# Kernel tuning notes

Measured on AMD Instinct MI355X. Metric: run time of the kernel, lower is better.

Reference implementation:

```python
import jax, jax.numpy as jnp
import numpy as np

N = 8192        # num_drugs
D_EMB = 256     # args.gcn_hidden3 (global encoder input)
D_FEAT = 256    # args.hidden_size (local encoder input)
H1 = H2 = H3 = 256  # args.ff_hidden1/2/3
LOG2 = float(np.log(2.0))
ADJ_DENSITY = 0.01


def _ff(x, w1, b1, w2, b2, w3, b3, ws, bs):
    # FF block: 3-layer ReLU MLP + linear shortcut (FF_local / FF_global)
    h = jax.nn.relu(x @ w1 + b1)
    h = jax.nn.relu(h @ w2 + b2)
    h = jax.nn.relu(h @ w3 + b3)
    return h + x @ ws + bs


def _lin_init(k, fan_in, fan_out):
    s = 1.0 / np.sqrt(fan_in)
    kw, kb = jax.random.split(k)
    w = jax.random.uniform(kw, (fan_in, fan_out), minval=-s, maxval=s, dtype=jnp.float32)
    b = jax.random.uniform(kb, (fan_out,), minval=-s, maxval=s, dtype=jnp.float32)
    return w, b


def setup_inputs() -> dict:
    key = jax.random.key(0)
    ks = jax.random.split(key, 11)
    g_w1, g_b1 = _lin_init(ks[0], D_EMB, H1)
    g_w2, g_b2 = _lin_init(ks[1], H1, H2)
    g_w3, g_b3 = _lin_init(ks[2], H2, H3)
    g_ws, g_bs = _lin_init(ks[3], D_EMB, H3)
    l_w1, l_b1 = _lin_init(ks[4], D_FEAT, H1)
    l_w2, l_b2 = _lin_init(ks[5], H1, H2)
    l_w3, l_b3 = _lin_init(ks[6], H2, H3)
    l_ws, l_bs = _lin_init(ks[7], D_FEAT, H3)
    embeddings = jax.random.normal(ks[8], (N, D_EMB), dtype=jnp.float32)
    features = jax.random.normal(ks[9], (N, D_FEAT), dtype=jnp.float32)
    adj_tensor = (jax.random.uniform(ks[10], (N, N)) < ADJ_DENSITY).astype(jnp.float32)
    return dict(embeddings=embeddings, features=features, adj_tensor=adj_tensor,
                num_drugs=N,
                g_w1=g_w1, g_b1=g_b1, g_w2=g_w2, g_b2=g_b2, g_w3=g_w3, g_b3=g_b3,
                g_ws=g_ws, g_bs=g_bs,
                l_w1=l_w1, l_b1=l_b1, l_w2=l_w2, l_b2=l_b2, l_w3=l_w3, l_b3=l_b3,
                l_ws=l_ws, l_bs=l_bs)


def reference(embeddings, features, adj_tensor,
              g_w1, g_b1, g_w2, g_b2, g_w3, g_b3, g_ws, g_bs,
              l_w1, l_b1, l_w2, l_b2, l_w3, l_b3, l_ws, l_bs,
              num_drugs):
    g_enc = _ff(embeddings, g_w1, g_b1, g_w2, g_b2, g_w3, g_b3, g_ws, g_bs)  # [N, H3]
    l_enc = _ff(features,   l_w1, l_b1, l_w2, l_b2, l_w3, l_b3, l_ws, l_bs)  # [N, H3]
    res = l_enc @ g_enc.T                      # [N, N] pairwise local-global scores
    pos_mask = adj_tensor
    neg_mask = 1.0 - adj_tensor
    # JSD estimator (as in InfoGraph/MIRACLE: mask applied BEFORE the expectation)
    p = res * pos_mask
    E_pos = jnp.sum(LOG2 - jax.nn.softplus(-p)) / num_drugs
    q = res * neg_mask
    E_neg = jnp.sum(jax.nn.softplus(-q) + q - LOG2) / (num_drugs * (num_drugs - 1))
    return E_neg - E_pos  # prior=False -> PRIOR term is 0
```

## Files before the change

kernel.cpp:

```cpp
#include <hip/hip_runtime.h>
#include <hip/hip_bf16.h>
#include <stdint.h>

typedef __bf16 bf16;
typedef __bf16 bf16x8 __attribute__((ext_vector_type(8)));
typedef float f32x4 __attribute__((ext_vector_type(4)));

#define N_DRUGS 8192
#define DIM 256
#define LOG2_C 0.6931471805599453f
#define W_POS (1.0f / 8192.0f)
#define W_NEG (1.0f / (8192.0f * 8191.0f))

__device__ inline void gload_lds16(const void* g, void* l) {
  __builtin_amdgcn_global_load_lds(
      (const __attribute__((address_space(1))) void*)g,
      (__attribute__((address_space(3))) void*)l, 16, 0, 0);
}

__device__ inline int swz(int row, int c) {
  return (c & ~7) | ((c ^ row) & 7);
}

__device__ inline float load_as_f32(const void* p, size_t idx, int dt_bf16) {
  return dt_bf16 ? (float)((const bf16*)p)[idx] : ((const float*)p)[idx];
}

__global__ void detect_dtype(const unsigned short* emb, int* flag) {
  int l = threadIdx.x & 63;
  unsigned short u = emb[2 * l];
  int e = (u >> 7) & 0xFF;
  int plausible = (e >= 96 && e <= 140) || (u == 0);
  unsigned long long m = __ballot(plausible);
  if (l == 0) *flag = (__popcll(m) >= 32) ? 1 : 0;
}

struct P8 { const void* p[8]; };

__global__ __launch_bounds__(256) void transpose_w(P8 srcs, bf16* wt,
                                                   const int* flag) {
  __shared__ bf16 t[32][33];
  const int dt = *flag;
  int m = blockIdx.z;
  const void* src = srcs.p[m];
  bf16* dst = wt + m * 65536;
  int bx = blockIdx.x * 32;
  int by = blockIdx.y * 32;
  int tx = threadIdx.x, ty = threadIdx.y;
#pragma unroll
  for (int i = 0; i < 32; i += 8)
    t[ty + i][tx] = (bf16)load_as_f32(src, (size_t)(by + ty + i) * DIM + bx + tx, dt);
  __syncthreads();
#pragma unroll
  for (int i = 0; i < 32; i += 8)
    dst[(bx + ty + i) * DIM + by + tx] = t[tx][ty + i];
}

struct FFArgs {
  const void *x, *b1, *b2, *b3, *bs;
  const bf16 *wt1, *wt2, *wt3, *wts;
  bf16* out;
};
struct FFBoth { FFArgs a[2]; };

__global__ __launch_bounds__(512) void ff_kernel(FFBoth both, const int* flag) {
  __shared__ __align__(16) bf16 xin[64 * 256];
  __shared__ __align__(16) bf16 cur[64 * 256];
  const FFArgs A = (blockIdx.y == 0) ? both.a[0] : both.a[1];
  const int dt = *flag;

  const int t = threadIdx.x;
  const int w = t >> 6, l = t & 63;
  const int lm = l & 15, lq = l >> 4;
  const int n0 = w * 32;
  const int r0 = blockIdx.x * 64;

  if (dt) {
#pragma unroll
    for (int it = 0; it < 4; ++it) {
      int ci = it * 512 + t, row = ci >> 5, c = ci & 31;
      *(bf16x8*)&xin[row * 256 + swz(row, c) * 8] =
          *(const bf16x8*)&((const bf16*)A.x)[(size_t)(r0 + row) * DIM + c * 8];
    }
  } else {
#pragma unroll
    for (int it = 0; it < 4; ++it) {
      int ci = it * 512 + t, row = ci >> 5, c = ci & 31;
      const float* src = &((const float*)A.x)[(size_t)(r0 + row) * DIM + c * 8];
      bf16x8 v;
#pragma unroll
      for (int e = 0; e < 8; ++e) v[e] = (bf16)src[e];
      *(bf16x8*)&xin[row * 256 + swz(row, c) * 8] = v;
    }
  }
  __syncthreads();

  f32x4 acc[4][2];
  const f32x4 fz = {0.f, 0.f, 0.f, 0.f};

  auto compute = [&](const bf16* src, const bf16* wt) {
#pragma unroll
    for (int i = 0; i < 4; ++i)
#pragma unroll
      for (int j = 0; j < 2; ++j) acc[i][j] = fz;
#pragma unroll
    for (int ks = 0; ks < 256; ks += 32) {
      bf16x8 af[4], bfr[2];
#pragma unroll
      for (int i = 0; i < 4; ++i) {
        int row = i * 16 + lm;
        af[i] = *(const bf16x8*)&src[row * 256 + swz(row, (ks >> 3) + lq) * 8];
      }
#pragma unroll
      for (int j = 0; j < 2; ++j) {
        int n = n0 + j * 16 + lm;
        bfr[j] = *(const bf16x8*)&wt[n * DIM + ks + lq * 8];
      }
#pragma unroll
      for (int i = 0; i < 4; ++i)
#pragma unroll
        for (int j = 0; j < 2; ++j)
          acc[i][j] = __builtin_amdgcn_mfma_f32_16x16x32_bf16(af[i], bfr[j],
                                                              acc[i][j], 0, 0, 0);
    }
  };

  auto store_relu = [&](const void* bias) {
    __syncthreads();
#pragma unroll
    for (int j = 0; j < 2; ++j) {
      int col = n0 + j * 16 + lm;
      float bj = load_as_f32(bias, col, dt);
      int cc = col >> 3, cw = col & 7;
#pragma unroll
      for (int i = 0; i < 4; ++i)
#pragma unroll
        for (int r = 0; r < 4; ++r) {
          int row = i * 16 + lq * 4 + r;
          float v = fmaxf(acc[i][j][r] + bj, 0.f);
          cur[row * 256 + swz(row, cc) * 8 + cw] = (bf16)v;
        }
    }
    __syncthreads();
  };

  compute(xin, A.wt1); store_relu(A.b1);
  compute(cur, A.wt2); store_relu(A.b2);
  compute(cur, A.wt3); store_relu(A.b3);
  compute(xin, A.wts);

  __syncthreads();
#pragma unroll
  for (int j = 0; j < 2; ++j) {
    int col = n0 + j * 16 + lm;
    float bj = load_as_f32(A.bs, col, dt);
    int cc = col >> 3, cw = col & 7;
#pragma unroll
    for (int i = 0; i < 4; ++i)
#pragma unroll
      for (int r = 0; r < 4; ++r) {
        int row = i * 16 + lq * 4 + r;
        float h3 = (float)cur[row * 256 + swz(row, cc) * 8 + cw];
        float v = acc[i][j][r] + bj + h3;
        xin[row * 256 + swz(row, cc) * 8 + cw] = (bf16)v;
      }
  }
  __syncthreads();
#pragma unroll
  for (int it = 0; it < 4; ++it) {
    int ci = it * 512 + t, row = ci >> 5, c = ci & 31;
    *(bf16x8*)&A.out[(size_t)(r0 + row) * DIM + c * 8] =
        *(const bf16x8*)&xin[row * 256 + swz(row, c) * 8];
  }
}

__global__ __launch_bounds__(256, 4) void gemm_reduce(const bf16* __restrict__ Lenc,
                                                      const bf16* __restrict__ Genc,
                                                      const void* __restrict__ adj,
                                                      float* accum, const int* flag) {
  __shared__ __align__(16) bf16 sb[2][2][128 * 32];
  __shared__ float red[4];

  const int dt = *flag;
  const int t = threadIdx.x;
  const int w = t >> 6, l = t & 63;
  const int wr = w >> 1, wc = w & 1;
  const int lm = l & 15, lq = l >> 4;
  const int row0 = blockIdx.y * 128;
  const int col0 = blockIdx.x * 128;

  auto stage = [&](int buf, int k) {
#pragma unroll
    for (int q = 0; q < 2; ++q) {
      int ci = q * 256 + t;
      int row = ci >> 2, c = ci & 3;
      int cg = c ^ (row & 3);
      gload_lds16(&Lenc[(size_t)(row0 + row) * DIM + k * 32 + cg * 8],
                  &sb[buf][0][(q * 256 + w * 64) * 8]);
      gload_lds16(&Genc[(size_t)(col0 + row) * DIM + k * 32 + cg * 8],
                  &sb[buf][1][(q * 256 + w * 64) * 8]);
    }
  };

  f32x4 acc[4][4];
  const f32x4 fz = {0.f, 0.f, 0.f, 0.f};
#pragma unroll
  for (int i = 0; i < 4; ++i)
#pragma unroll
    for (int j = 0; j < 4; ++j) acc[i][j] = fz;

  auto compute = [&](int buf) {
    bf16x8 af[4], bfr[4];
#pragma unroll
    for (int i = 0; i < 4; ++i) {
      int row = wr * 64 + i * 16 + lm;
      af[i] = *(const bf16x8*)&sb[buf][0][row * 32 + (lq ^ (row & 3)) * 8];
    }
#pragma unroll
    for (int j = 0; j < 4; ++j) {
      int row = wc * 64 + j * 16 + lm;
      bfr[j] = *(const bf16x8*)&sb[buf][1][row * 32 + (lq ^ (row & 3)) * 8];
    }
#pragma unroll
    for (int i = 0; i < 4; ++i)
#pragma unroll
      for (int j = 0; j < 4; ++j)
        acc[i][j] = __builtin_amdgcn_mfma_f32_16x16x32_bf16(af[i], bfr[j],
                                                            acc[i][j], 0, 0, 0);
  };

  stage(0, 0);
#pragma unroll
  for (int k = 0; k < 8; ++k) {
    const int cur = k & 1;
    if (k < 7) {
      stage(cur ^ 1, k + 1);
      asm volatile("s_waitcnt vmcnt(4)" ::: "memory");
    } else {
      asm volatile("s_waitcnt vmcnt(0)" ::: "memory");
    }
    __builtin_amdgcn_sched_barrier(0);
    __builtin_amdgcn_s_barrier();
    asm volatile("" ::: "memory");
    compute(cur);
    asm volatile("" ::: "memory");
    __builtin_amdgcn_s_barrier();
    asm volatile("" ::: "memory");
  }

  auto jsd = [&](float res, float a) {
    float s = fmaxf(res, 0.f) + __logf(1.f + __expf(-fabsf(res)));
    float vneg = (s - LOG2_C) * W_NEG;
    float vpos = (s - res - LOG2_C) * W_POS;
    return (a > 0.5f) ? vpos : vneg;
  };

  float lsum = 0.f;
  if (dt) {
    const bf16* gsrc = (const bf16*)adj +
        (size_t)(row0 + wr * 64) * N_DRUGS + col0 + wc * 64;
    bf16* wb = (bf16*)sb + w * 4096;
    int r8 = l >> 3, c8 = l & 7;
#pragma unroll
    for (int q = 0; q < 8; ++q)
      gload_lds16(gsrc + (size_t)(q * 8 + r8) * N_DRUGS + c8 * 8, wb + q * 512);
    asm volatile("s_waitcnt vmcnt(0)" ::: "memory");
    __builtin_amdgcn_sched_barrier(0);
#pragma unroll
    for (int i = 0; i < 4; ++i)
#pragma unroll
      for (int r = 0; r < 4; ++r) {
        int rc = i * 16 + lq * 4 + r;
#pragma unroll
        for (int j = 0; j < 4; ++j)
          lsum += jsd(acc[i][j][r], (float)wb[rc * 64 + j * 16 + lm]);
      }
  } else {
    const float* gsrc = (const float*)adj +
        (size_t)(row0 + wr * 64) * N_DRUGS + col0 + wc * 64;
    float* wfb = (float*)sb + w * 2048;
    auto issue = [&](int i) {
      float* cb = wfb + (i & 1) * 1024;
      const float* g = gsrc + (size_t)i * 16 * N_DRUGS;
#pragma unroll
      for (int q = 0; q < 4; ++q)
        gload_lds16(g + (size_t)(q * 4 + lq) * N_DRUGS + lm * 4, cb + q * 256);
    };
    issue(0);
    issue(1);
#pragma unroll
    for (int i = 0; i < 4; ++i) {
      if (i < 3) asm volatile("s_waitcnt vmcnt(4)" ::: "memory");
      else       asm volatile("s_waitcnt vmcnt(0)" ::: "memory");
      __builtin_amdgcn_sched_barrier(0);
      const float* cb = wfb + (i & 1) * 1024;
#pragma unroll
      for (int r = 0; r < 4; ++r) {
        int rc = lq * 4 + r;
#pragma unroll
        for (int j = 0; j < 4; ++j)
          lsum += jsd(acc[i][j][r], cb[rc * 64 + j * 16 + lm]);
      }
      if (i < 2) {
        asm volatile("s_waitcnt lgkmcnt(0)" ::: "memory");
        __builtin_amdgcn_sched_barrier(0);
        issue(i + 2);
      }
    }
  }

#pragma unroll
  for (int off = 32; off > 0; off >>= 1) lsum += __shfl_down(lsum, off, 64);
  if (l == 0) red[w] = lsum;
  __syncthreads();
  if (t == 0) atomicAdd(accum, red[0] + red[1] + red[2] + red[3]);
}

__global__ void finalize_k(const float* accum, unsigned int* out) {
  if (threadIdx.x == 0 && blockIdx.x == 0) {
    float v = *accum;
    union { bf16 h; unsigned short u; } cv;
    cv.h = (bf16)v;
    out[0] = ((unsigned int)cv.u << 16) | cv.u;
  }
}

extern "C" void kernel_launch(void* const* d_in, const int* in_sizes, int n_in,
                              void* d_out, int out_size, void* d_ws, size_t ws_size,
                              hipStream_t stream) {
  const void* embeddings = d_in[0];
  const void* features   = d_in[1];
  const void* adj        = d_in[2];

  char* ws = (char*)d_ws;
  float* accum = (float*)ws;
  int* flag = (int*)(ws + 64);
  bf16* wt   = (bf16*)(ws + 1024);
  bf16* genc = (bf16*)(ws + 1024 + 8 * 65536 * 2);
  bf16* lenc = (bf16*)(ws + 1024 + 8 * 65536 * 2 + (size_t)N_DRUGS * DIM * 2);

  hipMemsetAsync(accum, 0, sizeof(float), stream);

  detect_dtype<<<1, 64, 0, stream>>>((const unsigned short*)embeddings, flag);

  P8 srcs;
  srcs.p[0] = d_in[4];  srcs.p[1] = d_in[6];  srcs.p[2] = d_in[8];  srcs.p[3] = d_in[10];
  srcs.p[4] = d_in[12]; srcs.p[5] = d_in[14]; srcs.p[6] = d_in[16]; srcs.p[7] = d_in[18];
  transpose_w<<<dim3(8, 8, 8), dim3(32, 8), 0, stream>>>(srcs, wt, flag);

  FFBoth fb;
  fb.a[0] = FFArgs{embeddings, d_in[5], d_in[7], d_in[9], d_in[11],
                   wt + 0 * 65536, wt + 1 * 65536, wt + 2 * 65536, wt + 3 * 65536,
                   genc};
  fb.a[1] = FFArgs{features, d_in[13], d_in[15], d_in[17], d_in[19],
                   wt + 4 * 65536, wt + 5 * 65536, wt + 6 * 65536, wt + 7 * 65536,
                   lenc};
  ff_kernel<<<dim3(128, 2), 512, 0, stream>>>(fb, flag);

  gemm_reduce<<<dim3(64, 64), 256, 0, stream>>>(lenc, genc, adj, accum, flag);

  finalize_k<<<1, 64, 0, stream>>>(accum, (unsigned int*)d_out);
}
```

Baseline: 439.9 us.

## Pack adjacency into bitmap during FF kernel and read bits in GEMM epilogue

Adds a third block row to the FF kernel that streams the dense adjacency matrix and packs it into a 64-bit ballot bitmap in workspace. The GEMM epilogue then reads one 64-bit word per row segment from that bitmap instead of staging the dense fp32/bf16 adjacency tile through LDS. The adjacency is still read in full once, but now inside the otherwise underutilized FF launch (128x2 blocks), and the GEMM epilogue's memory traffic shrinks greatly. The cost is an extra bitmap write and read, a longer FF kernel, and scattered uncached-style 8-byte loads in the epilogue.

Measured after the change: 602.2 us. 36.9% more time.

```diff
diff --git a/kernel.cpp b/kernel.cpp
--- a/kernel.cpp
+++ b/kernel.cpp
@@ -63,14 +63,60 @@
 };
 struct FFBoth { FFArgs a[2]; };
 
-__global__ __launch_bounds__(512) void ff_kernel(FFBoth both, const int* flag) {
+__global__ __launch_bounds__(512) void ff_kernel(FFBoth both, const int* flag,
+                                                 const void* __restrict__ adj,
+                                                 unsigned long long* __restrict__ bm) {
   __shared__ __align__(16) bf16 xin[64 * 256];
   __shared__ __align__(16) bf16 cur[64 * 256];
-  const FFArgs A = (blockIdx.y == 0) ? both.a[0] : both.a[1];
   const int dt = *flag;
-
   const int t = threadIdx.x;
   const int w = t >> 6, l = t & 63;
+
+  if (blockIdx.y == 2) {
+    const int wid = blockIdx.x * 8 + w;
+    if (dt) {
+      const bf16* a = (const bf16*)adj;
+      const int IPW = (N_DRUGS * N_DRUGS / 512) / 1024;
+#pragma unroll 2
+      for (int it = 0; it < IPW; ++it) {
+        int g = wid * IPW + it;
+        const bf16x8 v = *(const bf16x8*)(a + (size_t)g * 512 + l * 8);
+        unsigned long long b0 = __ballot((float)v[0] > 0.5f);
+        unsigned long long b1 = __ballot((float)v[1] > 0.5f);
+        unsigned long long b2 = __ballot((float)v[2] > 0.5f);
+        unsigned long long b3 = __ballot((float)v[3] > 0.5f);
+        unsigned long long b4 = __ballot((float)v[4] > 0.5f);
+        unsigned long long b5 = __ballot((float)v[5] > 0.5f);
+        unsigned long long b6 = __ballot((float)v[6] > 0.5f);
+        unsigned long long b7 = __ballot((float)v[7] > 0.5f);
+        if (l < 8) {
+          unsigned long long x =
+              l < 4 ? (l < 2 ? (l == 0 ? b0 : b1) : (l == 2 ? b2 : b3))
+                    : (l < 6 ? (l == 4 ? b4 : b5) : (l == 6 ? b6 : b7));
+          bm[(size_t)g * 8 + l] = x;
+        }
+      }
+    } else {
+      const float* a = (const float*)adj;
+      const int IPW = (N_DRUGS * N_DRUGS / 256) / 1024;
+#pragma unroll 2
+      for (int it = 0; it < IPW; ++it) {
+        int g = wid * IPW + it;
+        f32x4 v = *(const f32x4*)(a + (size_t)g * 256 + l * 4);
+        unsigned long long b0 = __ballot(v[0] > 0.5f);
+        unsigned long long b1 = __ballot(v[1] > 0.5f);
+        unsigned long long b2 = __ballot(v[2] > 0.5f);
+        unsigned long long b3 = __ballot(v[3] > 0.5f);
+        if (l < 4) {
+          unsigned long long x = l < 2 ? (l == 0 ? b0 : b1) : (l == 2 ? b2 : b3);
+          bm[(size_t)g * 4 + l] = x;
+        }
+      }
+    }
+    return;
+  }
+
+  const FFArgs A = (blockIdx.y == 0) ? both.a[0] : both.a[1];
   const int lm = l & 15, lq = l >> 4;
   const int n0 = w * 32;
   const int r0 = blockIdx.x * 64;
@@ -176,7 +222,7 @@
 
 __global__ __launch_bounds__(256, 4) void gemm_reduce(const bf16* __restrict__ Lenc,
                                                       const bf16* __restrict__ Genc,
-                                                      const void* __restrict__ adj,
+                                                      const unsigned long long* __restrict__ bm,
                                                       float* accum, const int* flag) {
   __shared__ __align__(16) bf16 sb[2][2][128 * 32];
   __shared__ float red[4];
@@ -248,65 +294,44 @@
     asm volatile("" ::: "memory");
   }
 
-  auto jsd = [&](float res, float a) {
+  auto jsd = [&](float res, int pos) {
     float s = fmaxf(res, 0.f) + __logf(1.f + __expf(-fabsf(res)));
     float vneg = (s - LOG2_C) * W_NEG;
     float vpos = (s - res - LOG2_C) * W_POS;
-    return (a > 0.5f) ? vpos : vneg;
+    return pos ? vpos : vneg;
   };
 
   float lsum = 0.f;
+  const int colbase = col0 + wc * 64 + lm;
+  const int rbase = row0 + wr * 64 + lq * 4;
   if (dt) {
-    const bf16* gsrc = (const bf16*)adj +
-        (size_t)(row0 + wr * 64) * N_DRUGS + col0 + wc * 64;
-    bf16* wb = (bf16*)sb + w * 4096;
-    int r8 = l >> 3, c8 = l & 7;
-#pragma unroll
-    for (int q = 0; q < 8; ++q)
-      gload_lds16(gsrc + (size_t)(q * 8 + r8) * N_DRUGS + c8 * 8, wb + q * 512);
-    asm volatile("s_waitcnt vmcnt(0)" ::: "memory");
-    __builtin_amdgcn_sched_barrier(0);
+    const int cb = colbase >> 9;
+    const int kk = lm & 7;
+    const int lb = (colbase & 511) >> 3;
 #pragma unroll
     for (int i = 0; i < 4; ++i)
 #pragma unroll
       for (int r = 0; r < 4; ++r) {
-        int rc = i * 16 + lq * 4 + r;
+        int rc = rbase + i * 16 + r;
+        unsigned long long B = bm[((size_t)rc * 16 + cb) * 8 + kk];
 #pragma unroll
         for (int j = 0; j < 4; ++j)
-          lsum += jsd(acc[i][j][r], (float)wb[rc * 64 + j * 16 + lm]);
+          lsum += jsd(acc[i][j][r], (int)((B >> (lb + 2 * j)) & 1));
       }
   } else {
-    const float* gsrc = (const float*)adj +
-        (size_t)(row0 + wr * 64) * N_DRUGS + col0 + wc * 64;
-    float* wfb = (float*)sb + w * 2048;
-    auto issue = [&](int i) {
-      float* cb = wfb + (i & 1) * 1024;
-      const float* g = gsrc + (size_t)i * 16 * N_DRUGS;
-#pragma unroll
-      for (int q = 0; q < 4; ++q)
-        gload_lds16(g + (size_t)(q * 4 + lq) * N_DRUGS + lm * 4, cb + q * 256);
-    };
-    issue(0);
-    issue(1);
-#pragma unroll
-    for (int i = 0; i < 4; ++i) {
-      if (i < 3) asm volatile("s_waitcnt vmcnt(4)" ::: "memory");
-      else       asm volatile("s_waitcnt vmcnt(0)" ::: "memory");
-      __builtin_amdgcn_sched_barrier(0);
-      const float* cb = wfb + (i & 1) * 1024;
+    const int cb = colbase >> 8;
+    const int kk = lm & 3;
+    const int lb = (colbase & 255) >> 2;
+#pragma unroll
+    for (int i = 0; i < 4; ++i)
 #pragma unroll
       for (int r = 0; r < 4; ++r) {
-        int rc = lq * 4 + r;
+        int rc = rbase + i * 16 + r;
+        unsigned long long B = bm[((size_t)rc * 32 + cb) * 4 + kk];
 #pragma unroll
         for (int j = 0; j < 4; ++j)
-          lsum += jsd(acc[i][j][r], cb[rc * 64 + j * 16 + lm]);
-      }
-      if (i < 2) {
-        asm volatile("s_waitcnt lgkmcnt(0)" ::: "memory");
-        __builtin_amdgcn_sched_barrier(0);
-        issue(i + 2);
-      }
-    }
+          lsum += jsd(acc[i][j][r], (int)((B >> (lb + 4 * j)) & 1));
+      }
   }
 
 #pragma unroll
@@ -338,6 +363,7 @@
   bf16* wt   = (bf16*)(ws + 1024);
   bf16* genc = (bf16*)(ws + 1024 + 8 * 65536 * 2);
   bf16* lenc = (bf16*)(ws + 1024 + 8 * 65536 * 2 + (size_t)N_DRUGS * DIM * 2);
+  unsigned long long* bitmap = (unsigned long long*)(ws + 16 * 1024 * 1024);
 
   hipMemsetAsync(accum, 0, sizeof(float), stream);
 
@@ -355,9 +381,9 @@
   fb.a[1] = FFArgs{features, d_in[13], d_in[15], d_in[17], d_in[19],
                    wt + 4 * 65536, wt + 5 * 65536, wt + 6 * 65536, wt + 7 * 65536,
                    lenc};
-  ff_kernel<<<dim3(128, 2), 512, 0, stream>>>(fb, flag);
-
-  gemm_reduce<<<dim3(64, 64), 256, 0, stream>>>(lenc, genc, adj, accum, flag);
+  ff_kernel<<<dim3(128, 3), 512, 0, stream>>>(fb, flag, adj, bitmap);
+
+  gemm_reduce<<<dim3(64, 64), 256, 0, stream>>>(lenc, genc, bitmap, accum, flag);
 
   finalize_k<<<1, 64, 0, stream>>>(accum, (unsigned int*)d_out);
 }
```

## Shrink gemm tiles to 64x64, prefetch adjacency at kernel start, spread atomics

Applied to the files above, without the earlier changes.

The pairwise GEMM+JSD kernel now uses 64x64 output tiles with four times as many blocks. It issues the block's whole adjacency tile load into a dedicated swizzled LDS buffer before the K loop, so the adjacency read overlaps the MFMA work instead of running after it. The single global atomic accumulator is split into 64 padded slots that finalize sums, which reduces atomic contention. The trade-offs are that Lenc/Genc get re-read four times as often, each wave does less MFMA work per load, and the workspace layout is shifted.

Measured after the change: 474.8 us. 1.08x slower.

```diff
diff --git a/kernel.cpp b/kernel.cpp
--- a/kernel.cpp
+++ b/kernel.cpp
@@ -178,7 +178,8 @@
                                                       const bf16* __restrict__ Genc,
                                                       const void* __restrict__ adj,
                                                       float* accum, const int* flag) {
-  __shared__ __align__(16) bf16 sb[2][2][128 * 32];
+  __shared__ __align__(16) bf16 sb[2][2][64 * 32];
+  __shared__ __align__(16) char adjL[16384];
   __shared__ float red[4];
 
   const int dt = *flag;
@@ -186,45 +187,63 @@
   const int w = t >> 6, l = t & 63;
   const int wr = w >> 1, wc = w & 1;
   const int lm = l & 15, lq = l >> 4;
-  const int row0 = blockIdx.y * 128;
-  const int col0 = blockIdx.x * 128;
-
-  auto stage = [&](int buf, int k) {
+  const int row0 = blockIdx.y * 64;
+  const int col0 = blockIdx.x * 64;
+
+  if (dt) {
+    const bf16* gsrc = (const bf16*)adj + (size_t)row0 * N_DRUGS + col0;
 #pragma unroll
     for (int q = 0; q < 2; ++q) {
       int ci = q * 256 + t;
-      int row = ci >> 2, c = ci & 3;
-      int cg = c ^ (row & 3);
-      gload_lds16(&Lenc[(size_t)(row0 + row) * DIM + k * 32 + cg * 8],
-                  &sb[buf][0][(q * 256 + w * 64) * 8]);
-      gload_lds16(&Genc[(size_t)(col0 + row) * DIM + k * 32 + cg * 8],
-                  &sb[buf][1][(q * 256 + w * 64) * 8]);
-    }
-  };
-
-  f32x4 acc[4][4];
+      int row = ci >> 3, c = ci & 7;
+      int cg = c ^ (row & 7);
+      gload_lds16(gsrc + (size_t)row * N_DRUGS + cg * 8,
+                  (bf16*)adjL + (q * 256 + w * 64) * 8);
+    }
+  } else {
+    const float* gsrc = (const float*)adj + (size_t)row0 * N_DRUGS + col0;
+#pragma unroll
+    for (int q = 0; q < 4; ++q) {
+      int ci = q * 256 + t;
+      int row = ci >> 4, c = ci & 15;
+      int cg = c ^ (row & 15);
+      gload_lds16(gsrc + (size_t)row * N_DRUGS + cg * 4,
+                  (float*)adjL + (q * 256 + w * 64) * 4);
+    }
+  }
+
+  auto stage = [&](int buf, int k) {
+    int row = t >> 2, c = t & 3;
+    int cg = c ^ (row & 3);
+    gload_lds16(&Lenc[(size_t)(row0 + row) * DIM + k * 32 + cg * 8],
+                &sb[buf][0][(w * 64) * 8]);
+    gload_lds16(&Genc[(size_t)(col0 + row) * DIM + k * 32 + cg * 8],
+                &sb[buf][1][(w * 64) * 8]);
+  };
+
+  f32x4 acc[2][2];
   const f32x4 fz = {0.f, 0.f, 0.f, 0.f};
 #pragma unroll
-  for (int i = 0; i < 4; ++i)
-#pragma unroll
-    for (int j = 0; j < 4; ++j) acc[i][j] = fz;
+  for (int i = 0; i < 2; ++i)
+#pragma unroll
+    for (int j = 0; j < 2; ++j) acc[i][j] = fz;
 
   auto compute = [&](int buf) {
-    bf16x8 af[4], bfr[4];
-#pragma unroll
-    for (int i = 0; i < 4; ++i) {
-      int row = wr * 64 + i * 16 + lm;
+    bf16x8 af[2], bfr[2];
+#pragma unroll
+    for (int i = 0; i < 2; ++i) {
+      int row = wr * 32 + i * 16 + lm;
       af[i] = *(const bf16x8*)&sb[buf][0][row * 32 + (lq ^ (row & 3)) * 8];
     }
 #pragma unroll
-    for (int j = 0; j < 4; ++j) {
-      int row = wc * 64 + j * 16 + lm;
+    for (int j = 0; j < 2; ++j) {
+      int row = wc * 32 + j * 16 + lm;
       bfr[j] = *(const bf16x8*)&sb[buf][1][row * 32 + (lq ^ (row & 3)) * 8];
     }
 #pragma unroll
-    for (int i = 0; i < 4; ++i)
-#pragma unroll
-      for (int j = 0; j < 4; ++j)
+    for (int i = 0; i < 2; ++i)
+#pragma unroll
+      for (int j = 0; j < 2; ++j)
         acc[i][j] = __builtin_amdgcn_mfma_f32_16x16x32_bf16(af[i], bfr[j],
                                                             acc[i][j], 0, 0, 0);
   };
@@ -235,7 +254,7 @@
     const int cur = k & 1;
     if (k < 7) {
       stage(cur ^ 1, k + 1);
-      asm volatile("s_waitcnt vmcnt(4)" ::: "memory");
+      asm volatile("s_waitcnt vmcnt(2)" ::: "memory");
     } else {
       asm volatile("s_waitcnt vmcnt(0)" ::: "memory");
     }
@@ -257,68 +276,50 @@
 
   float lsum = 0.f;
   if (dt) {
-    const bf16* gsrc = (const bf16*)adj +
-        (size_t)(row0 + wr * 64) * N_DRUGS + col0 + wc * 64;
-    bf16* wb = (bf16*)sb + w * 4096;
-    int r8 = l >> 3, c8 = l & 7;
-#pragma unroll
-    for (int q = 0; q < 8; ++q)
-      gload_lds16(gsrc + (size_t)(q * 8 + r8) * N_DRUGS + c8 * 8, wb + q * 512);
-    asm volatile("s_waitcnt vmcnt(0)" ::: "memory");
-    __builtin_amdgcn_sched_barrier(0);
-#pragma unroll
-    for (int i = 0; i < 4; ++i)
+    const bf16* ab = (const bf16*)adjL;
+#pragma unroll
+    for (int i = 0; i < 2; ++i)
 #pragma unroll
       for (int r = 0; r < 4; ++r) {
-        int rc = i * 16 + lq * 4 + r;
-#pragma unroll
-        for (int j = 0; j < 4; ++j)
-          lsum += jsd(acc[i][j][r], (float)wb[rc * 64 + j * 16 + lm]);
+        int rc = wr * 32 + i * 16 + lq * 4 + r;
+#pragma unroll
+        for (int j = 0; j < 2; ++j) {
+          int col = wc * 32 + j * 16 + lm;
+          int slot = (col >> 3) ^ (rc & 7);
+          float a = (float)ab[rc * 64 + slot * 8 + (col & 7)];
+          lsum += jsd(acc[i][j][r], a);
+        }
       }
   } else {
-    const float* gsrc = (const float*)adj +
-        (size_t)(row0 + wr * 64) * N_DRUGS + col0 + wc * 64;
-    float* wfb = (float*)sb + w * 2048;
-    auto issue = [&](int i) {
-      float* cb = wfb + (i & 1) * 1024;
-      const float* g = gsrc + (size_t)i * 16 * N_DRUGS;
-#pragma unroll
-      for (int q = 0; q < 4; ++q)
-        gload_lds16(g + (size_t)(q * 4 + lq) * N_DRUGS + lm * 4, cb + q * 256);
-    };
-    issue(0);
-    issue(1);
-#pragma unroll
-    for (int i = 0; i < 4; ++i) {
-      if (i < 3) asm volatile("s_waitcnt vmcnt(4)" ::: "memory");
-      else       asm volatile("s_waitcnt vmcnt(0)" ::: "memory");
-      __builtin_amdgcn_sched_barrier(0);
-      const float* cb = wfb + (i & 1) * 1024;
+    const float* ab = (const float*)adjL;
+#pragma unroll
+    for (int i = 0; i < 2; ++i)
 #pragma unroll
       for (int r = 0; r < 4; ++r) {
-        int rc = lq * 4 + r;
-#pragma unroll
-        for (int j = 0; j < 4; ++j)
-          lsum += jsd(acc[i][j][r], cb[rc * 64 + j * 16 + lm]);
-      }
-      if (i < 2) {
-        asm volatile("s_waitcnt lgkmcnt(0)" ::: "memory");
-        __builtin_amdgcn_sched_barrier(0);
-        issue(i + 2);
-      }
-    }
+        int rc = wr * 32 + i * 16 + lq * 4 + r;
+#pragma unroll
+        for (int j = 0; j < 2; ++j) {
+          int col = wc * 32 + j * 16 + lm;
+          int slot = (col >> 2) ^ (rc & 15);
+          float a = ab[rc * 64 + slot * 4 + (col & 3)];
+          lsum += jsd(acc[i][j][r], a);
+        }
+      }
   }
 
 #pragma unroll
   for (int off = 32; off > 0; off >>= 1) lsum += __shfl_down(lsum, off, 64);
   if (l == 0) red[w] = lsum;
   __syncthreads();
-  if (t == 0) atomicAdd(accum, red[0] + red[1] + red[2] + red[3]);
+  if (t == 0)
+    atomicAdd(&accum[(blockIdx.x & 63) * 16],
+              red[0] + red[1] + red[2] + red[3]);
 }
 
 __global__ void finalize_k(const float* accum, unsigned int* out) {
   if (threadIdx.x == 0 && blockIdx.x == 0) {
-    float v = *accum;
+    float v = 0.f;
+    for (int i = 0; i < 64; ++i) v += accum[i * 16];
     union { bf16 h; unsigned short u; } cv;
     cv.h = (bf16)v;
     out[0] = ((unsigned int)cv.u << 16) | cv.u;
@@ -334,12 +335,12 @@
 
   char* ws = (char*)d_ws;
   float* accum = (float*)ws;
-  int* flag = (int*)(ws + 64);
-  bf16* wt   = (bf16*)(ws + 1024);
-  bf16* genc = (bf16*)(ws + 1024 + 8 * 65536 * 2);
-  bf16* lenc = (bf16*)(ws + 1024 + 8 * 65536 * 2 + (size_t)N_DRUGS * DIM * 2);
-
-  hipMemsetAsync(accum, 0, sizeof(float), stream);
+  int* flag = (int*)(ws + 8192);
+  bf16* wt   = (bf16*)(ws + 16384);
+  bf16* genc = (bf16*)(ws + 2 * 1024 * 1024);
+  bf16* lenc = (bf16*)(ws + 6 * 1024 * 1024);
+
+  hipMemsetAsync(accum, 0, 64 * 16 * sizeof(float), stream);
 
   detect_dtype<<<1, 64, 0, stream>>>((const unsigned short*)embeddings, flag);
 
@@ -357,7 +358,7 @@
                    lenc};
   ff_kernel<<<dim3(128, 2), 512, 0, stream>>>(fb, flag);
 
-  gemm_reduce<<<dim3(64, 64), 256, 0, stream>>>(lenc, genc, adj, accum, flag);
+  gemm_reduce<<<dim3(128, 128), 256, 0, stream>>>(lenc, genc, adj, accum, flag);
 
   finalize_k<<<1, 64, 0, stream>>>(accum, (unsigned int*)d_out);
 }
```
